# Performance work log

Measured on AMD Instinct MI355X. Metric: run time of the kernel, lower is better.

The kernel has to match this reference:

```python
import jax, jax.numpy as jnp
import numpy as np

N_LEVELS = 8
N_FEATS = 8            # features per level
BASE_RES = 16
PER_LEVEL_SCALE = 1.2599210739135742
LOG2_HASHMAP = 19
TABLE_PAD = 8192       # padded per-level table rows (>= max level size 6568)
N_POINTS = 262144


def _level_params(l):
    # tcnn: scale = base * s^l - 1 ; res = ceil(scale)+1 ; size = min(2^19, round_up(res^2, 8))
    scale = BASE_RES * (PER_LEVEL_SCALE ** l) - 1.0
    res = int(np.ceil(scale)) + 1
    size = min(1 << LOG2_HASHMAP, ((res * res + 7) // 8) * 8)
    return float(scale), res, size


def hashgrid_encode(x, table):
    """x: [N,2] in [0,1), table: [L, TABLE_PAD, F]. Returns [N, L*F]."""
    outs = []
    for l in range(N_LEVELS):
        scale, res, size = _level_params(l)
        pos = x * jnp.float32(scale) + jnp.float32(0.5)
        pg = jnp.floor(pos)
        frac = pos - pg
        pg = pg.astype(jnp.int32)
        # Smoothstep interpolation weights: t^2 (3 - 2t)
        w = frac * frac * (3.0 - 2.0 * frac)          # [N,2]
        feat = jnp.zeros((x.shape[0], N_FEATS), dtype=table.dtype)
        for dx in (0, 1):
            wx = w[:, 0] if dx else 1.0 - w[:, 0]
            for dy in (0, 1):
                wy = w[:, 1] if dy else 1.0 - w[:, 1]
                # dense grid index (all levels here fit the hashmap), modulo level size as in tcnn
                idx = ((pg[:, 0] + dx) + (pg[:, 1] + dy) * res) % size
                feat = feat + (wx * wy)[:, None] * table[l, idx]  # irregular gather
        outs.append(feat)
    return jnp.concatenate(outs, axis=-1)  # [N, 64]


def mlp(enc, W0, W1, W2, W3):
    h = jax.nn.relu(enc @ W0)
    h = jax.nn.relu(h @ W1)
    h = jax.nn.relu(h @ W2)
    return h @ W3  # linear output activation


def setup_inputs() -> dict:
    key = jax.random.key(0)
    ks = jax.random.split(key, 6)
    x = jax.random.uniform(ks[0], (N_POINTS, 2), dtype=jnp.float32)
    # tcnn initializes grid params ~ uniform(-1e-4, 1e-4); small values
    table = jax.random.normal(ks[1], (N_LEVELS, TABLE_PAD, N_FEATS), dtype=jnp.float32) * 1e-2
    W0 = jax.random.normal(ks[2], (64, 256), dtype=jnp.float32) * (1.0 / np.sqrt(64))
    W1 = jax.random.normal(ks[3], (256, 256), dtype=jnp.float32) * (1.0 / np.sqrt(256))
    W2 = jax.random.normal(ks[4], (256, 256), dtype=jnp.float32) * (1.0 / np.sqrt(256))
    W3 = jax.random.normal(ks[5], (256, 1), dtype=jnp.float32) * (1.0 / np.sqrt(256))
    return {"x": x, "table": table, "W0": W0, "W1": W1, "W2": W2, "W3": W3}


def reference(x, table, W0, W1, W2, W3):
    enc = hashgrid_encode(x, table)
    return mlp(enc, W0, W1, W2, W3)  # [N, 1]
```

## Files before the change

kernel.cpp:

```cpp
#include <hip/hip_runtime.h>
#include <cmath>


#define N_LEVELS 8
#define TABLE_PAD 8192
#define TILE_M 64
#define ACT_STRIDE 264
#define ENC_STRIDE 72

typedef __attribute__((ext_vector_type(8))) short short8;
typedef __attribute__((ext_vector_type(4))) float float4v;

struct LevelParams {
  float scale[N_LEVELS];
  int   res[N_LEVELS];
  int   size[N_LEVELS];
};

__device__ __forceinline__ unsigned short f2bf(float f) {
  unsigned int u = __float_as_uint(f);
  u += 0x7fffu + ((u >> 16) & 1u);
  return (unsigned short)(u >> 16);
}
__device__ __forceinline__ float bf2f(unsigned short h) {
  return __uint_as_float(((unsigned int)h) << 16);
}
__device__ __forceinline__ unsigned int pack2bf(float a, float b) {
  a = a > 0.f ? a : 0.f;
  b = b > 0.f ? b : 0.f;
  return (unsigned int)f2bf(a) | ((unsigned int)f2bf(b) << 16);
}

__global__ void pack_weights_kernel(const float* __restrict__ W0,
                                    const float* __restrict__ W1,
                                    const float* __restrict__ W2,
                                    unsigned short* __restrict__ Wp) {
  int tid = blockIdx.x * blockDim.x + threadIdx.x;
  const float* src;
  int base, e;
  if (tid < 16384)        { src = W0; base = 0;     e = tid;         }
  else if (tid < 81920)   { src = W1; base = 16384; e = tid - 16384; }
  else if (tid < 147456)  { src = W2; base = 81920; e = tid - 81920; }
  else return;
  int ki = e & 31;
  int n  = (e >> 5) & 255;
  int kb = e >> 13;
  Wp[base + e] = f2bf(src[(kb * 32 + ki) * 256 + n]);
}

__global__ __launch_bounds__(512, 4) void neural_field_kernel(
    const float* __restrict__ x,
    const float* __restrict__ table,
    const unsigned short* __restrict__ Wp,
    const float* __restrict__ W3,
    float* __restrict__ out,
    LevelParams P) {
  __shared__ unsigned short bufE[TILE_M * ENC_STRIDE];
  __shared__ unsigned short bufA[TILE_M * ACT_STRIDE];
  __shared__ unsigned short bufB[TILE_M * ACT_STRIDE];

  const int t  = threadIdx.x;
  const int g0 = blockIdx.x * TILE_M;

  {
    int p = t & 63;
    int l = t >> 6;
    float2 xy = ((const float2*)x)[g0 + p];
    float scale = P.scale[l];
    int res = P.res[l], size = P.size[l];
    float posx = xy.x * scale + 0.5f;
    float posy = xy.y * scale + 0.5f;
    float pgx = floorf(posx), pgy = floorf(posy);
    float fx = posx - pgx, fy = posy - pgy;
    float wx = fx * fx * (3.0f - 2.0f * fx);
    float wy = fy * fy * (3.0f - 2.0f * fy);
    int px = (int)pgx, py = (int)pgy;
    float acc[8] = {0, 0, 0, 0, 0, 0, 0, 0};
    for (int dy = 0; dy < 2; ++dy) {
      float wyv = dy ? wy : 1.0f - wy;
      for (int dx = 0; dx < 2; ++dx) {
        float wgt = (dx ? wx : 1.0f - wx) * wyv;
        int idx = (px + dx) + (py + dy) * res;
        if (idx >= size) idx -= size;
        const float4* tp =
            (const float4*)(table + ((size_t)l * TABLE_PAD + idx) * 8);
        float4 t0 = tp[0], t1 = tp[1];
        acc[0] += wgt * t0.x; acc[1] += wgt * t0.y;
        acc[2] += wgt * t0.z; acc[3] += wgt * t0.w;
        acc[4] += wgt * t1.x; acc[5] += wgt * t1.y;
        acc[6] += wgt * t1.z; acc[7] += wgt * t1.w;
      }
    }
    union { unsigned short s[8]; short8 v; } u;
    for (int j = 0; j < 8; ++j) u.s[j] = f2bf(acc[j]);
    *(short8*)&bufE[p * ENC_STRIDE + l * 8] = u.v;
  }

  const int lane  = t & 63;
  const int w     = t >> 6;
  const int l15   = lane & 15;
  const int quad  = lane >> 4;
  const int wbase = w * 32;

  auto run_layer = [&](const unsigned short* inb, int in_stride,
                       unsigned short* outb, const unsigned short* Wpl,
                       int KB) {
    float4v acc[2][4];
    for (int ft = 0; ft < 2; ++ft)
      for (int pt = 0; pt < 4; ++pt)
        acc[ft][pt] = (float4v){0.f, 0.f, 0.f, 0.f};

    const unsigned short* ap[4];
    for (int pt = 0; pt < 4; ++pt)
      ap[pt] = &inb[(pt * 16 + l15) * in_stride + quad * 8];
    const unsigned short* wp = &Wpl[(wbase + l15) * 32 + quad * 8];

#pragma unroll
    for (int kb = 0; kb < KB; ++kb) {
      short8 wf[2], af[4];
      for (int ft = 0; ft < 2; ++ft)
        wf[ft] = *(const short8*)(wp + kb * 8192 + ft * 512);
      for (int pt = 0; pt < 4; ++pt)
        af[pt] = *(const short8*)(ap[pt] + kb * 32);
      for (int ft = 0; ft < 2; ++ft)
        for (int pt = 0; pt < 4; ++pt)
          acc[ft][pt] = __builtin_amdgcn_mfma_f32_16x16x32_bf16(
              wf[ft], af[pt], acc[ft][pt], 0, 0, 0);
    }

    for (int ft = 0; ft < 2; ++ft) {
      int n0 = wbase + ft * 16 + quad * 4;
      for (int pt = 0; pt < 4; ++pt) {
        int m = pt * 16 + l15;
        uint2 pk;
        pk.x = pack2bf(acc[ft][pt][0], acc[ft][pt][1]);
        pk.y = pack2bf(acc[ft][pt][2], acc[ft][pt][3]);
        *(uint2*)&outb[m * ACT_STRIDE + n0] = pk;
      }
    }
  };

  __syncthreads();
  run_layer(bufE, ENC_STRIDE, bufA, Wp,         2);
  __syncthreads();
  run_layer(bufA, ACT_STRIDE, bufB, Wp + 16384, 8);
  __syncthreads();
  run_layer(bufB, ACT_STRIDE, bufA, Wp + 81920, 8);
  __syncthreads();

  {
    int p = t >> 3;
    int q = t & 7;
    float s = 0.f;
    for (int c8 = 0; c8 < 4; ++c8) {
      int chunk = q * 4 + c8;
      short8 h = *(const short8*)&bufA[p * ACT_STRIDE + chunk * 8];
      float4 w0v = *(const float4*)(W3 + chunk * 8);
      float4 w1v = *(const float4*)(W3 + chunk * 8 + 4);
      s += bf2f((unsigned short)h[0]) * w0v.x;
      s += bf2f((unsigned short)h[1]) * w0v.y;
      s += bf2f((unsigned short)h[2]) * w0v.z;
      s += bf2f((unsigned short)h[3]) * w0v.w;
      s += bf2f((unsigned short)h[4]) * w1v.x;
      s += bf2f((unsigned short)h[5]) * w1v.y;
      s += bf2f((unsigned short)h[6]) * w1v.z;
      s += bf2f((unsigned short)h[7]) * w1v.w;
    }
    s += __shfl_xor(s, 1);
    s += __shfl_xor(s, 2);
    s += __shfl_xor(s, 4);
    if (q == 0) out[g0 + p] = s;
  }
}

extern "C" void kernel_launch(void* const* d_in, const int* in_sizes, int n_in,
                              void* d_out, int out_size, void* d_ws,
                              size_t ws_size, hipStream_t stream) {
  const float* x     = (const float*)d_in[0];
  const float* table = (const float*)d_in[1];
  const float* W0    = (const float*)d_in[2];
  const float* W1    = (const float*)d_in[3];
  const float* W2    = (const float*)d_in[4];
  const float* W3    = (const float*)d_in[5];
  float* out = (float*)d_out;
  int N = in_sizes[0] / 2;

  unsigned short* Wp = (unsigned short*)d_ws;

  LevelParams P;
  const double c = 1.2599210739135742;
  double m = 1.0;
  for (int l = 0; l < N_LEVELS; ++l) {
    double scale_d = 16.0 * m - 1.0;
    int res = (int)std::ceil(scale_d) + 1;
    long long sz = ((long long)res * res + 7) / 8 * 8;
    if (sz > (1LL << 19)) sz = 1LL << 19;
    P.scale[l] = (float)scale_d;
    P.res[l]   = res;
    P.size[l]  = (int)sz;
    m *= c;
  }

  hipLaunchKernelGGL(pack_weights_kernel, dim3(576), dim3(256), 0, stream,
                     W0, W1, W2, Wp);
  hipLaunchKernelGGL(neural_field_kernel, dim3(N / TILE_M), dim3(512), 0,
                     stream, x, table, Wp, W3, out, P);
}
```

Baseline: 190.0 us.

## Switch to 32x32x16 MFMA, prefetch operands, fuse final layer into third

Repacks the weights for 16-wide K blocks and replaces the 16x16x32 MFMA tiling with 32x32x16 MFMAs, two accumulators per wave. Each K step now loads the next weight and activation fragments one step ahead to overlap loads with matrix math. The 256->1 output layer is folded into the third layer's epilogue: ReLU outputs are dotted with W3 in registers and reduced through a small shared buffer, so the last activation tile is never written or reread in bf16. This cuts LDS traffic and instruction count, at the cost of more accumulator registers and a different fp32 summation order for the output.

```diff
diff --git a/kernel.cpp b/kernel.cpp
--- a/kernel.cpp
+++ b/kernel.cpp
@@ -9,7 +9,7 @@
 #define ENC_STRIDE 72
 
 typedef __attribute__((ext_vector_type(8))) short short8;
-typedef __attribute__((ext_vector_type(4))) float float4v;
+typedef __attribute__((ext_vector_type(16))) float float16v;
 
 struct LevelParams {
   float scale[N_LEVELS];
@@ -21,9 +21,6 @@
   unsigned int u = __float_as_uint(f);
   u += 0x7fffu + ((u >> 16) & 1u);
   return (unsigned short)(u >> 16);
-}
-__device__ __forceinline__ float bf2f(unsigned short h) {
-  return __uint_as_float(((unsigned int)h) << 16);
 }
 __device__ __forceinline__ unsigned int pack2bf(float a, float b) {
   a = a > 0.f ? a : 0.f;
@@ -42,10 +39,12 @@
   else if (tid < 81920)   { src = W1; base = 16384; e = tid - 16384; }
   else if (tid < 147456)  { src = W2; base = 81920; e = tid - 81920; }
   else return;
-  int ki = e & 31;
-  int n  = (e >> 5) & 255;
-  int kb = e >> 13;
-  Wp[base + e] = f2bf(src[(kb * 32 + ki) * 256 + n]);
+  int ki = e & 15;
+  int n  = (e >> 4) & 255;
+  int kb = e >> 12;
+  unsigned int u = __float_as_uint(src[(kb * 16 + ki) * 256 + n]);
+  u += 0x7fffu + ((u >> 16) & 1u);
+  Wp[base + e] = (unsigned short)(u >> 16);
 }
 
 __global__ __launch_bounds__(512, 4) void neural_field_kernel(
@@ -61,6 +60,14 @@
 
   const int t  = threadIdx.x;
   const int g0 = blockIdx.x * TILE_M;
+
+  const int lane  = t & 63;
+  const int w     = t >> 6;
+  const int l31   = lane & 31;
+  const int h8    = lane >> 5;
+  const int wbase = w * 32;
+
+  const int woff = (wbase + l31) * 16 + h8 * 8;
 
   {
     int p = t & 63;
@@ -96,80 +103,92 @@
     *(short8*)&bufE[p * ENC_STRIDE + l * 8] = u.v;
   }
 
-  const int lane  = t & 63;
-  const int w     = t >> 6;
-  const int l15   = lane & 15;
-  const int quad  = lane >> 4;
-  const int wbase = w * 32;
-
   auto run_layer = [&](const unsigned short* inb, int in_stride,
                        unsigned short* outb, const unsigned short* Wpl,
-                       int KB) {
-    float4v acc[2][4];
-    for (int ft = 0; ft < 2; ++ft)
-      for (int pt = 0; pt < 4; ++pt)
-        acc[ft][pt] = (float4v){0.f, 0.f, 0.f, 0.f};
-
-    const unsigned short* ap[4];
-    for (int pt = 0; pt < 4; ++pt)
-      ap[pt] = &inb[(pt * 16 + l15) * in_stride + quad * 8];
-    const unsigned short* wp = &Wpl[(wbase + l15) * 32 + quad * 8];
+                       int KB, short8 wf0, bool fuse_final,
+                       float* fsum) {
+    float16v acc[2];
+    for (int j = 0; j < 16; ++j) { acc[0][j] = 0.f; acc[1][j] = 0.f; }
+
+    const unsigned short* ap0 = &inb[l31 * in_stride + h8 * 8];
+    const unsigned short* ap1 = ap0 + 32 * in_stride;
+    const unsigned short* wp  = Wpl + woff;
+
+    float w3f[16];
+    if (fuse_final) {
+      for (int q = 0; q < 4; ++q) {
+        float4 wv = *(const float4*)(W3 + wbase + 8 * q + 4 * h8);
+        w3f[4 * q + 0] = wv.x; w3f[4 * q + 1] = wv.y;
+        w3f[4 * q + 2] = wv.z; w3f[4 * q + 3] = wv.w;
+      }
+    }
+
+    short8 af0[2];
+    af0[0] = *(const short8*)(ap0);
+    af0[1] = *(const short8*)(ap1);
 
 #pragma unroll
     for (int kb = 0; kb < KB; ++kb) {
-      short8 wf[2], af[4];
-      for (int ft = 0; ft < 2; ++ft)
-        wf[ft] = *(const short8*)(wp + kb * 8192 + ft * 512);
-      for (int pt = 0; pt < 4; ++pt)
-        af[pt] = *(const short8*)(ap[pt] + kb * 32);
-      for (int ft = 0; ft < 2; ++ft)
-        for (int pt = 0; pt < 4; ++pt)
-          acc[ft][pt] = __builtin_amdgcn_mfma_f32_16x16x32_bf16(
-              wf[ft], af[pt], acc[ft][pt], 0, 0, 0);
-    }
-
-    for (int ft = 0; ft < 2; ++ft) {
-      int n0 = wbase + ft * 16 + quad * 4;
-      for (int pt = 0; pt < 4; ++pt) {
-        int m = pt * 16 + l15;
-        uint2 pk;
-        pk.x = pack2bf(acc[ft][pt][0], acc[ft][pt][1]);
-        pk.y = pack2bf(acc[ft][pt][2], acc[ft][pt][3]);
-        *(uint2*)&outb[m * ACT_STRIDE + n0] = pk;
-      }
+      short8 wf1, af1[2];
+      int kn = (kb + 1 < KB) ? kb + 1 : kb;
+      wf1    = *(const short8*)(wp + kn * 4096);
+      af1[0] = *(const short8*)(ap0 + kn * 16);
+      af1[1] = *(const short8*)(ap1 + kn * 16);
+
+      acc[0] = __builtin_amdgcn_mfma_f32_32x32x16_bf16(wf0, af0[0], acc[0],
+                                                       0, 0, 0);
+      acc[1] = __builtin_amdgcn_mfma_f32_32x32x16_bf16(wf0, af0[1], acc[1],
+                                                       0, 0, 0);
+      wf0 = wf1; af0[0] = af1[0]; af0[1] = af1[1];
+    }
+
+    if (!fuse_final) {
+      for (int pt = 0; pt < 2; ++pt) {
+        int m = pt * 32 + l31;
+        for (int q = 0; q < 4; ++q) {
+          int n0 = wbase + 8 * q + 4 * h8;
+          uint2 pk;
+          pk.x = pack2bf(acc[pt][4 * q + 0], acc[pt][4 * q + 1]);
+          pk.y = pack2bf(acc[pt][4 * q + 2], acc[pt][4 * q + 3]);
+          *(uint2*)&outb[m * ACT_STRIDE + n0] = pk;
+        }
+      }
+    } else {
+      float part0 = 0.f, part1 = 0.f;
+      for (int j = 0; j < 16; ++j) {
+        float v0 = acc[0][j]; v0 = v0 > 0.f ? v0 : 0.f;
+        float v1 = acc[1][j]; v1 = v1 > 0.f ? v1 : 0.f;
+        part0 += v0 * w3f[j];
+        part1 += v1 * w3f[j];
+      }
+      part0 += __shfl_xor(part0, 32);
+      part1 += __shfl_xor(part1, 32);
+      float val = h8 ? part1 : part0;
+      fsum[lane * 9 + w] = val;
     }
   };
 
-  __syncthreads();
-  run_layer(bufE, ENC_STRIDE, bufA, Wp,         2);
-  __syncthreads();
-  run_layer(bufA, ACT_STRIDE, bufB, Wp + 16384, 8);
-  __syncthreads();
-  run_layer(bufB, ACT_STRIDE, bufA, Wp + 81920, 8);
+  float* fsum = (float*)bufE;
+
+  short8 wf = *(const short8*)(Wp + woff);
+  __syncthreads();
+  run_layer(bufE, ENC_STRIDE, bufA, Wp, 4, wf, false, fsum);
+  wf = *(const short8*)(Wp + 16384 + woff);
+  __syncthreads();
+  run_layer(bufA, ACT_STRIDE, bufB, Wp + 16384, 16, wf, false, fsum);
+  wf = *(const short8*)(Wp + 81920 + woff);
+  __syncthreads();
+  run_layer(bufB, ACT_STRIDE, nullptr, Wp + 81920, 16, wf, true, fsum);
   __syncthreads();
 
   {
     int p = t >> 3;
     int q = t & 7;
-    float s = 0.f;
-    for (int c8 = 0; c8 < 4; ++c8) {
-      int chunk = q * 4 + c8;
-      short8 h = *(const short8*)&bufA[p * ACT_STRIDE + chunk * 8];
-      float4 w0v = *(const float4*)(W3 + chunk * 8);
-      float4 w1v = *(const float4*)(W3 + chunk * 8 + 4);
-      s += bf2f((unsigned short)h[0]) * w0v.x;
-      s += bf2f((unsigned short)h[1]) * w0v.y;
-      s += bf2f((unsigned short)h[2]) * w0v.z;
-      s += bf2f((unsigned short)h[3]) * w0v.w;
-      s += bf2f((unsigned short)h[4]) * w1v.x;
-      s += bf2f((unsigned short)h[5]) * w1v.y;
-      s += bf2f((unsigned short)h[6]) * w1v.z;
-      s += bf2f((unsigned short)h[7]) * w1v.w;
-    }
-    s += __shfl_xor(s, 1);
-    s += __shfl_xor(s, 2);
-    s += __shfl_xor(s, 4);
-    if (q == 0) out[g0 + p] = s;
+    float v = fsum[p * 9 + q];
+    v += __shfl_xor(v, 1);
+    v += __shfl_xor(v, 2);
+    v += __shfl_xor(v, 4);
+    if (q == 0) out[g0 + p] = v;
   }
 }
 
```

Measured after the change: 163.7 us. -13.8%, faster.
